# Kernel tuning notes

Hardware: AMD Instinct MI355X
Metric: run time of the kernel (lower is better)

The kernel has to match this reference:

```python
import jax, jax.numpy as jnp
import numpy as np
from itertools import combinations

NUM_FIELDS = 39
EMBED_DIM = 16
BATCH = 8192
EPS = 1e-5


def _pairs(n):
    idx = np.array(list(combinations(range(n), 2)), dtype=np.int32)  # [P, 2]
    cols, rows = idx[:, 0], idx[:, 1]
    return rows, cols


def setup_inputs() -> dict:
    key = jax.random.key(0)
    k1, k2 = jax.random.split(key)
    rows, cols = _pairs(NUM_FIELDS)
    P = rows.shape[0]  # 741
    x = jax.random.normal(k1, (BATCH, NUM_FIELDS, EMBED_DIM), dtype=jnp.float32)
    # edge_weights ~ U(0.599, 0.601) as in torch init
    edge_weights = jax.random.uniform(k2, (P,), dtype=jnp.float32,
                                      minval=0.599, maxval=0.601)
    gamma = jnp.ones((P,), dtype=jnp.float32)
    beta = jnp.zeros((P,), dtype=jnp.float32)
    return {"x": x, "edge_weights": edge_weights, "gamma": gamma,
            "beta": beta, "rows": jnp.asarray(rows), "cols": jnp.asarray(cols)}


def reference(x, edge_weights, gamma, beta, rows, cols):
    # gather field-pair embeddings: [B, P, D]
    left = x[:, rows, :]
    right = x[:, cols, :]
    inter = jnp.sum(left * right, axis=-1)  # [B, P]
    # BatchNorm1d (training mode, biased variance over batch)
    mean = jnp.mean(inter, axis=0)
    var = jnp.mean(jnp.square(inter - mean), axis=0)
    norm = (inter - mean) * jax.lax.rsqrt(var + EPS) * gamma + beta
    fm_out = jnp.sum(norm * edge_weights, axis=-1, keepdims=True)  # [B, 1]
    return fm_out
```

## Files before the change

### kernel.cpp

```cpp
#include <hip/hip_runtime.h>

#define NF      39
#define ED      16
#define PAIRS   741
#define PADP    768
#define ROWPAD  20
#define SROW    (NF*ROWPAD)
#define SAMP    8
#define BATCH   8192
#define NBLK    (BATCH/SAMP)
#define F4_PER_SAMPLE (NF*ED/4)
#define EPS     1e-5f

__global__ __launch_bounds__(256) void stats_k(
    const float* __restrict__ x, const int* __restrict__ rows,
    const int* __restrict__ cols, float* __restrict__ S1,
    float* __restrict__ S2, int repMask)
{
    __shared__ float lds[SAMP * SROW];
    const int t = threadIdx.x;
    const size_t base = (size_t)blockIdx.x * SAMP;
    const float4* xg = (const float4*)(x + base * (NF * ED));

    for (int u = t; u < SAMP * F4_PER_SAMPLE; u += 256) {
        int s = u / F4_PER_SAMPLE;
        int f = u - s * F4_PER_SAMPLE;
        float4 v = xg[u];
        *(float4*)&lds[s * SROW + (f >> 2) * ROWPAD + ((f & 3) << 2)] = v;
    }
    __syncthreads();

    const int r = blockIdx.x & repMask;
    for (int p = t; p < PAIRS; p += 256) {
        const int ci = cols[p] * ROWPAD;
        const int rj = rows[p] * ROWPAD;
        float s1 = 0.f, s2 = 0.f;
        #pragma unroll
        for (int s = 0; s < SAMP; ++s) {
            const float4* A  = (const float4*)&lds[s * SROW + ci];
            const float4* Bv = (const float4*)&lds[s * SROW + rj];
            float v = 0.f;
            #pragma unroll
            for (int k = 0; k < 4; ++k) {
                float4 a = A[k], b = Bv[k];
                v = fmaf(a.x, b.x, v); v = fmaf(a.y, b.y, v);
                v = fmaf(a.z, b.z, v); v = fmaf(a.w, b.w, v);
            }
            s1 += v;
            s2 = fmaf(v, v, s2);
        }
        atomicAdd(&S1[r * PADP + p], s1);
        atomicAdd(&S2[r * PADP + p], s2);
    }
}

__global__ __launch_bounds__(256) void out_k(
    const float* __restrict__ x, const float* __restrict__ ew,
    const float* __restrict__ gamma, const float* __restrict__ beta,
    const int* __restrict__ rows, const int* __restrict__ cols,
    const float* __restrict__ S1, const float* __restrict__ S2,
    float* __restrict__ out, int rep)
{
    __shared__ float lds[SAMP * SROW];
    __shared__ float cred[4];
    __shared__ float sred[4][SAMP];
    const int t = threadIdx.x;
    const size_t base = (size_t)blockIdx.x * SAMP;
    const float4* xg = (const float4*)(x + base * (NF * ED));

    for (int u = t; u < SAMP * F4_PER_SAMPLE; u += 256) {
        int s = u / F4_PER_SAMPLE;
        int f = u - s * F4_PER_SAMPLE;
        float4 v = xg[u];
        *(float4*)&lds[s * SROW + (f >> 2) * ROWPAD + ((f & 3) << 2)] = v;
    }
    __syncthreads();

    float wacc[SAMP];
    #pragma unroll
    for (int s = 0; s < SAMP; ++s) wacc[s] = 0.f;
    float cloc = 0.f;

    for (int p = t; p < PAIRS; p += 256) {
        const int ci = cols[p] * ROWPAD;
        const int rj = rows[p] * ROWPAD;

        float s1 = 0.f, s2 = 0.f;
        for (int r = 0; r < rep; ++r) {
            s1 += S1[r * PADP + p];
            s2 += S2[r * PADP + p];
        }
        const float mean = s1 * (1.f / BATCH);
        const float var  = fmaf(-mean, mean, s2 * (1.f / BATCH));
        const float rs   = 1.f / sqrtf(var + EPS);
        const float g    = gamma[p] * rs;
        const float w    = ew[p];
        const float a    = g * w;
        cloc += (beta[p] - mean * g) * w;

        #pragma unroll
        for (int s = 0; s < SAMP; ++s) {
            const float4* A  = (const float4*)&lds[s * SROW + ci];
            const float4* Bv = (const float4*)&lds[s * SROW + rj];
            float v = 0.f;
            #pragma unroll
            for (int k = 0; k < 4; ++k) {
                float4 a4 = A[k], b4 = Bv[k];
                v = fmaf(a4.x, b4.x, v); v = fmaf(a4.y, b4.y, v);
                v = fmaf(a4.z, b4.z, v); v = fmaf(a4.w, b4.w, v);
            }
            wacc[s] = fmaf(a, v, wacc[s]);
        }
    }

    #pragma unroll
    for (int m = 32; m >= 1; m >>= 1) {
        cloc += __shfl_xor(cloc, m, 64);
        #pragma unroll
        for (int s = 0; s < SAMP; ++s) wacc[s] += __shfl_xor(wacc[s], m, 64);
    }
    const int wv = t >> 6, ln = t & 63;
    if (ln == 0) {
        cred[wv] = cloc;
        #pragma unroll
        for (int s = 0; s < SAMP; ++s) sred[wv][s] = wacc[s];
    }
    __syncthreads();
    if (t < SAMP) {
        float c = cred[0] + cred[1] + cred[2] + cred[3];
        float o = sred[0][t] + sred[1][t] + sred[2][t] + sred[3][t];
        out[base + t] = o + c;
    }
}

extern "C" void kernel_launch(void* const* d_in, const int* in_sizes, int n_in,
                              void* d_out, int out_size, void* d_ws, size_t ws_size,
                              hipStream_t stream)
{
    (void)in_sizes; (void)n_in; (void)out_size;
    const float* x     = (const float*)d_in[0];
    const float* ew    = (const float*)d_in[1];
    const float* gamma = (const float*)d_in[2];
    const float* beta  = (const float*)d_in[3];
    const int*   rows  = (const int*)d_in[4];
    const int*   cols  = (const int*)d_in[5];
    float* out = (float*)d_out;

    int rep = 8;
    while (rep > 1 && (size_t)(2 * rep * PADP * sizeof(float)) > ws_size) rep >>= 1;
    float* S1 = (float*)d_ws;
    float* S2 = S1 + rep * PADP;

    hipMemsetAsync(d_ws, 0, 2 * (size_t)rep * PADP * sizeof(float), stream);
    stats_k<<<NBLK, 256, 0, stream>>>(x, rows, cols, S1, S2, rep - 1);
    out_k<<<NBLK, 256, 0, stream>>>(x, ew, gamma, beta, rows, cols, S1, S2, out, rep);
}
```

Baseline: 104.5 us.

## Compute pair dot products as 4x4 register tiles over field blocks

Both kernels now split the 39x39 upper triangle of field pairs into 55 tiles of 4x4 fields per sample. Each thread loads 8 field vectors from LDS and computes 16 dot products, where before it loaded two vectors per pair. This reuses each loaded vector across four pairs and stops reading the rows/cols index arrays, assuming the standard combinations ordering. The stats kernel writes the dot results to an LDS buffer before the per-pair reduction. The out kernel precomputes per-pair coefficients into LDS before the tile pass. The tile loop covers only 440 work items, so half the threads idle on the second pass, and diagonal and padded tiles compute some unused products.

```diff
diff --git a/kernel.cpp b/kernel.cpp
--- a/kernel.cpp
+++ b/kernel.cpp
@@ -6,130 +6,174 @@
 #define PADP    768
 #define ROWPAD  20
 #define SROW    (NF*ROWPAD)
+#define IPAD    772
 #define SAMP    8
 #define BATCH   8192
 #define NBLK    (BATCH/SAMP)
-#define F4_PER_SAMPLE (NF*ED/4)
+#define F4S     (NF*ED/4)
 #define EPS     1e-5f
+#define REP     8
+
+__device__ __forceinline__ float dot4(float4 a, float4 b) {
+    float v = a.x * b.x;
+    v = fmaf(a.y, b.y, v);
+    v = fmaf(a.z, b.z, v);
+    v = fmaf(a.w, b.w, v);
+    return v;
+}
+
+__device__ __forceinline__ void tile_decode(int tile, int& tc, int& tr) {
+    int rem = tile;
+    tc = 0;
+    while (rem >= 10 - tc) { rem -= 10 - tc; ++tc; }
+    tr = tc + rem;
+}
+
+__device__ __forceinline__ void tile_dots(const float* sb, int tc, int tr,
+                                          float acc[4][4]) {
+    int cOff[4], rOff[4];
+    #pragma unroll
+    for (int i = 0; i < 4; ++i) cOff[i] = min(4 * tc + i, NF - 1) * ROWPAD;
+    #pragma unroll
+    for (int j = 0; j < 4; ++j) rOff[j] = min(4 * tr + j, NF - 1) * ROWPAD;
+    #pragma unroll
+    for (int i = 0; i < 4; ++i)
+        #pragma unroll
+        for (int j = 0; j < 4; ++j) acc[i][j] = 0.f;
+    #pragma unroll
+    for (int k = 0; k < 4; ++k) {
+        float4 a[4], b[4];
+        #pragma unroll
+        for (int i = 0; i < 4; ++i) a[i] = *(const float4*)&sb[cOff[i] + 4 * k];
+        #pragma unroll
+        for (int j = 0; j < 4; ++j) b[j] = *(const float4*)&sb[rOff[j] + 4 * k];
+        #pragma unroll
+        for (int i = 0; i < 4; ++i)
+            #pragma unroll
+            for (int j = 0; j < 4; ++j)
+                acc[i][j] += dot4(a[i], b[j]);
+    }
+}
 
 __global__ __launch_bounds__(256) void stats_k(
-    const float* __restrict__ x, const int* __restrict__ rows,
-    const int* __restrict__ cols, float* __restrict__ S1,
-    float* __restrict__ S2, int repMask)
+    const float* __restrict__ x, float* __restrict__ S1, float* __restrict__ S2)
 {
-    __shared__ float lds[SAMP * SROW];
+    __shared__ float stage[SAMP * SROW];
+    __shared__ float ibuf[SAMP * IPAD];
     const int t = threadIdx.x;
     const size_t base = (size_t)blockIdx.x * SAMP;
     const float4* xg = (const float4*)(x + base * (NF * ED));
 
-    for (int u = t; u < SAMP * F4_PER_SAMPLE; u += 256) {
-        int s = u / F4_PER_SAMPLE;
-        int f = u - s * F4_PER_SAMPLE;
+    for (int u = t; u < SAMP * F4S; u += 256) {
+        int s = u / F4S, f = u - s * F4S;
         float4 v = xg[u];
-        *(float4*)&lds[s * SROW + (f >> 2) * ROWPAD + ((f & 3) << 2)] = v;
+        *(float4*)&stage[s * SROW + (f >> 2) * ROWPAD + ((f & 3) << 2)] = v;
     }
     __syncthreads();
 
-    const int r = blockIdx.x & repMask;
+    for (int u = t; u < 55 * SAMP; u += 256) {
+        const int s = u & 7;
+        int tc, tr;
+        tile_decode(u >> 3, tc, tr);
+        float acc[4][4];
+        tile_dots(&stage[s * SROW], tc, tr, acc);
+        const int sbase = s * IPAD;
+        #pragma unroll
+        for (int i = 0; i < 4; ++i) {
+            const int c = 4 * tc + i;
+            const int pb = 38 * c - (c * (c - 1)) / 2 - c - 1;
+            #pragma unroll
+            for (int j = 0; j < 4; ++j) {
+                const int r = 4 * tr + j;
+                if (c < r && r < NF) ibuf[sbase + pb + r] = acc[i][j];
+            }
+        }
+    }
+    __syncthreads();
+
+    const int rp = (blockIdx.x & (REP - 1)) * PADP;
     for (int p = t; p < PAIRS; p += 256) {
-        const int ci = cols[p] * ROWPAD;
-        const int rj = rows[p] * ROWPAD;
         float s1 = 0.f, s2 = 0.f;
         #pragma unroll
         for (int s = 0; s < SAMP; ++s) {
-            const float4* A  = (const float4*)&lds[s * SROW + ci];
-            const float4* Bv = (const float4*)&lds[s * SROW + rj];
-            float v = 0.f;
-            #pragma unroll
-            for (int k = 0; k < 4; ++k) {
-                float4 a = A[k], b = Bv[k];
-                v = fmaf(a.x, b.x, v); v = fmaf(a.y, b.y, v);
-                v = fmaf(a.z, b.z, v); v = fmaf(a.w, b.w, v);
-            }
-            s1 += v;
-            s2 = fmaf(v, v, s2);
+            float v = ibuf[s * IPAD + p];
+            s1 += v; s2 = fmaf(v, v, s2);
         }
-        atomicAdd(&S1[r * PADP + p], s1);
-        atomicAdd(&S2[r * PADP + p], s2);
+        atomicAdd(&S1[rp + p], s1);
+        atomicAdd(&S2[rp + p], s2);
     }
 }
 
 __global__ __launch_bounds__(256) void out_k(
-    const float* __restrict__ x, const float* __restrict__ ew,
+    const float* __restrict__ x, const float* __restrict__ S1,
+    const float* __restrict__ S2, const float* __restrict__ ew,
     const float* __restrict__ gamma, const float* __restrict__ beta,
-    const int* __restrict__ rows, const int* __restrict__ cols,
-    const float* __restrict__ S1, const float* __restrict__ S2,
-    float* __restrict__ out, int rep)
+    float* __restrict__ out)
 {
-    __shared__ float lds[SAMP * SROW];
+    __shared__ float stage[SAMP * SROW];
+    __shared__ float aS[PADP];
     __shared__ float cred[4];
     __shared__ float sred[4][SAMP];
     const int t = threadIdx.x;
     const size_t base = (size_t)blockIdx.x * SAMP;
     const float4* xg = (const float4*)(x + base * (NF * ED));
 
-    for (int u = t; u < SAMP * F4_PER_SAMPLE; u += 256) {
-        int s = u / F4_PER_SAMPLE;
-        int f = u - s * F4_PER_SAMPLE;
+    for (int u = t; u < SAMP * F4S; u += 256) {
+        int s = u / F4S, f = u - s * F4S;
         float4 v = xg[u];
-        *(float4*)&lds[s * SROW + (f >> 2) * ROWPAD + ((f & 3) << 2)] = v;
+        *(float4*)&stage[s * SROW + (f >> 2) * ROWPAD + ((f & 3) << 2)] = v;
     }
+
+    float cl = 0.f;
+    for (int p = t; p < PADP; p += 256) {
+        float a = 0.f;
+        if (p < PAIRS) {
+            float s1 = 0.f, s2 = 0.f;
+            #pragma unroll
+            for (int r = 0; r < REP; ++r) {
+                s1 += S1[r * PADP + p];
+                s2 += S2[r * PADP + p];
+            }
+            const float mean = s1 * (1.f / BATCH);
+            const float var  = fmaf(-mean, mean, s2 * (1.f / BATCH));
+            const float g    = gamma[p] / sqrtf(var + EPS);
+            const float w    = ew[p];
+            a = w * g;
+            cl = fmaf(beta[p] - mean * g, w, cl);
+        }
+        aS[p] = a;
+    }
+    #pragma unroll
+    for (int m = 32; m; m >>= 1) cl += __shfl_xor(cl, m, 64);
+    if ((t & 63) == 0) cred[t >> 6] = cl;
     __syncthreads();
+    const float Cv = cred[0] + cred[1] + cred[2] + cred[3];
 
-    float wacc[SAMP];
-    #pragma unroll
-    for (int s = 0; s < SAMP; ++s) wacc[s] = 0.f;
-    float cloc = 0.f;
-
-    for (int p = t; p < PAIRS; p += 256) {
-        const int ci = cols[p] * ROWPAD;
-        const int rj = rows[p] * ROWPAD;
-
-        float s1 = 0.f, s2 = 0.f;
-        for (int r = 0; r < rep; ++r) {
-            s1 += S1[r * PADP + p];
-            s2 += S2[r * PADP + p];
-        }
-        const float mean = s1 * (1.f / BATCH);
-        const float var  = fmaf(-mean, mean, s2 * (1.f / BATCH));
-        const float rs   = 1.f / sqrtf(var + EPS);
-        const float g    = gamma[p] * rs;
-        const float w    = ew[p];
-        const float a    = g * w;
-        cloc += (beta[p] - mean * g) * w;
-
+    float wsum = 0.f;
+    for (int u = t; u < 55 * SAMP; u += 256) {
+        const int s = u & 7;
+        int tc, tr;
+        tile_decode(u >> 3, tc, tr);
+        float acc[4][4];
+        tile_dots(&stage[s * SROW], tc, tr, acc);
         #pragma unroll
-        for (int s = 0; s < SAMP; ++s) {
-            const float4* A  = (const float4*)&lds[s * SROW + ci];
-            const float4* Bv = (const float4*)&lds[s * SROW + rj];
-            float v = 0.f;
+        for (int i = 0; i < 4; ++i) {
+            const int c = 4 * tc + i;
+            const int pb = 38 * c - (c * (c - 1)) / 2 - c - 1;
             #pragma unroll
-            for (int k = 0; k < 4; ++k) {
-                float4 a4 = A[k], b4 = Bv[k];
-                v = fmaf(a4.x, b4.x, v); v = fmaf(a4.y, b4.y, v);
-                v = fmaf(a4.z, b4.z, v); v = fmaf(a4.w, b4.w, v);
+            for (int j = 0; j < 4; ++j) {
+                const int r = 4 * tr + j;
+                if (c < r && r < NF) wsum = fmaf(aS[pb + r], acc[i][j], wsum);
             }
-            wacc[s] = fmaf(a, v, wacc[s]);
         }
     }
 
     #pragma unroll
-    for (int m = 32; m >= 1; m >>= 1) {
-        cloc += __shfl_xor(cloc, m, 64);
-        #pragma unroll
-        for (int s = 0; s < SAMP; ++s) wacc[s] += __shfl_xor(wacc[s], m, 64);
-    }
-    const int wv = t >> 6, ln = t & 63;
-    if (ln == 0) {
-        cred[wv] = cloc;
-        #pragma unroll
-        for (int s = 0; s < SAMP; ++s) sred[wv][s] = wacc[s];
-    }
+    for (int m = 8; m < 64; m <<= 1) wsum += __shfl_xor(wsum, m, 64);
+    if ((t & 63) < 8) sred[t >> 6][t & 7] = wsum;
     __syncthreads();
     if (t < SAMP) {
-        float c = cred[0] + cred[1] + cred[2] + cred[3];
-        float o = sred[0][t] + sred[1][t] + sred[2][t] + sred[3][t];
-        out[base + t] = o + c;
+        out[base + t] = sred[0][t] + sred[1][t] + sred[2][t] + sred[3][t] + Cv;
     }
 }
 
@@ -137,21 +181,17 @@
                               void* d_out, int out_size, void* d_ws, size_t ws_size,
                               hipStream_t stream)
 {
-    (void)in_sizes; (void)n_in; (void)out_size;
+    (void)in_sizes; (void)n_in; (void)out_size; (void)ws_size;
     const float* x     = (const float*)d_in[0];
     const float* ew    = (const float*)d_in[1];
     const float* gamma = (const float*)d_in[2];
     const float* beta  = (const float*)d_in[3];
-    const int*   rows  = (const int*)d_in[4];
-    const int*   cols  = (const int*)d_in[5];
     float* out = (float*)d_out;
 
-    int rep = 8;
-    while (rep > 1 && (size_t)(2 * rep * PADP * sizeof(float)) > ws_size) rep >>= 1;
     float* S1 = (float*)d_ws;
-    float* S2 = S1 + rep * PADP;
+    float* S2 = S1 + REP * PADP;
 
-    hipMemsetAsync(d_ws, 0, 2 * (size_t)rep * PADP * sizeof(float), stream);
-    stats_k<<<NBLK, 256, 0, stream>>>(x, rows, cols, S1, S2, rep - 1);
-    out_k<<<NBLK, 256, 0, stream>>>(x, ew, gamma, beta, rows, cols, S1, S2, out, rep);
+    hipMemsetAsync(d_ws, 0, 2 * REP * PADP * sizeof(float), stream);
+    stats_k<<<NBLK, 256, 0, stream>>>(x, S1, S2);
+    out_k<<<NBLK, 256, 0, stream>>>(x, S1, S2, ew, gamma, beta, out);
 }
```

New measurement: 103.4 us, median of 2. Within noise of the previous version (-1.0%).
